# Optimization experiments

Hardware: AMD Instinct MI355X
Metric: run time of the kernel (lower is better)

The kernel has to match this reference:

```python
import jax, jax.numpy as jnp
import numpy as np

B, N, DIM, EMB_H, EXP, K = 1, 1024, 64, 64, 4, 16


def setup_inputs() -> dict:
    key = jax.random.key(0)
    ks = jax.random.split(key, 12)
    s = lambda k, *shape: jax.random.normal(k, shape, dtype=jnp.float32) * 0.05
    return {
        "x": jax.random.normal(ks[0], (B, N, DIM), dtype=jnp.float32),
        "pos": jax.random.normal(ks[1], (B, N, 3), dtype=jnp.float32),
        "Wq": s(ks[2], DIM, DIM),
        "Wk": s(ks[3], DIM, DIM),
        "Wv": s(ks[4], DIM, DIM),
        "P1": s(ks[5], 3, EMB_H), "pb1": jnp.zeros((EMB_H,), jnp.float32),
        "P2": s(ks[6], EMB_H, DIM), "pb2": jnp.zeros((DIM,), jnp.float32),
        "A1": s(ks[7], DIM, DIM * EXP), "ab1": jnp.zeros((DIM * EXP,), jnp.float32),
        "A2": s(ks[8], DIM * EXP, DIM), "ab2": jnp.zeros((DIM,), jnp.float32),
        "nneighbors": K,
    }


def reference(x, pos, Wq, Wk, Wv, P1, pb1, P2, pb2, A1, ab1, A2, ab2, nneighbors):
    b, n, d = x.shape
    q = x @ Wq            # [b,n,d]
    k = x @ Wk
    v = x @ Wv
    qk_rel = q[:, :, None, :] - k[:, None, :, :]          # [b,n,n,d]
    rel_pos = pos[:, :, None, :] - pos[:, None, :, :]      # [b,n,n,3]
    rel_pos_emb = jax.nn.relu(rel_pos @ P1 + pb1) @ P2 + pb2  # [b,n,n,d]
    # kNN selection on euclidean distance (smallest nneighbors)
    rel_dist = jnp.linalg.norm(rel_pos, axis=-1)           # [b,n,n]
    _, idx = jax.lax.top_k(-rel_dist, nneighbors)          # [b,n,K]
    bidx = jnp.arange(b)[:, None, None]
    v_g = v[bidx, idx]                                     # [b,n,K,d]
    qk_g = jnp.take_along_axis(qk_rel, idx[..., None], axis=2)        # [b,n,K,d]
    rpe_g = jnp.take_along_axis(rel_pos_emb, idx[..., None], axis=2)  # [b,n,K,d]
    v_g = v_g + rpe_g
    sim = jax.nn.relu((qk_g + rpe_g) @ A1 + ab1) @ A2 + ab2  # [b,n,K,d]
    attn = jax.nn.softmax(sim, axis=-2)                      # softmax over neighbors
    agg = jnp.sum(attn * v_g, axis=2)                        # [b,n,d]
    return agg
```

## Files before the change

### kernel.cpp

```cpp
#include <hip/hip_runtime.h>

#define NPTS 1024
#define DIMD 64
#define KNN  16
#define HID  256
#define EMBH 64

typedef short short8 __attribute__((ext_vector_type(8)));
typedef float f32x4  __attribute__((ext_vector_type(4)));

__device__ __forceinline__ short f2bf(float x) {
    unsigned u = __float_as_uint(x);
    unsigned r = (u + 0x7fffu + ((u >> 16) & 1u)) >> 16;
    return (short)r;
}
__device__ __forceinline__ float bf2f(short s) {
    return __uint_as_float(((unsigned)(unsigned short)s) << 16);
}

__device__ __host__ __forceinline__ int frag_off(int K, int k, int n) {
    int T = n >> 4, c = k >> 5, q = (k >> 3) & 3, j = k & 7;
    int lane = (q << 4) | (n & 15);
    return ((T * (K >> 5) + c) * 64 + lane) * 8 + j;
}

#define A1HI 0
#define A1LO 16384
#define A2HI 32768
#define A2LO 49152
#define WKHI 65536
#define WKLO 69632
#define WVHI 73728
#define WVLO 77824
#define P2HI 81920
#define P2LO 86016
#define WS_SHORTS 90112

__global__ __launch_bounds__(256) void prep_weights(
    const float* __restrict__ A1, const float* __restrict__ A2,
    const float* __restrict__ Wk, const float* __restrict__ Wv,
    const float* __restrict__ P2, short* __restrict__ ws)
{
    int e = blockIdx.x * 256 + threadIdx.x;
    float v; int hi_base, lo_base, off;
    if (e < 16384)      { int k = e >> 8, n = e & 255;               v = A1[e];
                          hi_base = A1HI; lo_base = A1LO; off = frag_off(64,  k, n); }
    else if (e < 32768) { int t = e - 16384; int k = t >> 6, n = t & 63; v = A2[t];
                          hi_base = A2HI; lo_base = A2LO; off = frag_off(256, k, n); }
    else if (e < 36864) { int t = e - 32768; int k = t >> 6, n = t & 63; v = Wk[t];
                          hi_base = WKHI; lo_base = WKLO; off = frag_off(64,  k, n); }
    else if (e < 40960) { int t = e - 36864; int k = t >> 6, n = t & 63; v = Wv[t];
                          hi_base = WVHI; lo_base = WVLO; off = frag_off(64,  k, n); }
    else if (e < 45056) { int t = e - 40960; int k = t >> 6, n = t & 63; v = P2[t];
                          hi_base = P2HI; lo_base = P2LO; off = frag_off(64,  k, n); }
    else return;
    short h = f2bf(v);
    short l = f2bf(v - bf2f(h));
    ws[hi_base + off] = h;
    ws[lo_base + off] = l;
}

__global__ __launch_bounds__(256, 4) void ptl_fused(
    const float* __restrict__ x,  const float* __restrict__ pos,
    const float* __restrict__ Wq,
    const float* __restrict__ P1, const float* __restrict__ pb1,
    const float* __restrict__ pb2,
    const float* __restrict__ ab1, const float* __restrict__ ab2,
    const short* __restrict__ ws,
    float* __restrict__ out)
{
    __shared__ __align__(16) float s_big[16 * 260];
    __shared__ __align__(16) float s_es[16 * 68];
    __shared__ __align__(16) float s_xn[16 * 68];
    __shared__ __align__(16) float s_h[16 * 68];
    __shared__ __align__(16) float s_vg[16 * 68];
    __shared__ float s_q[DIMD];
    __shared__ int s_idx[KNN];

    const int i   = blockIdx.x;
    const int tid = threadIdx.x;
    const int lane = tid & 63;
    const int w    = tid >> 6;
    const int q4   = lane >> 4;
    const int col  = lane & 15;

    const float px = pos[i*3+0], py = pos[i*3+1], pz = pos[i*3+2];

    #pragma unroll
    for (int u = 0; u < 4; u++) {
        int j = tid + 256 * u;
        float dx = __fsub_rn(px, pos[j*3+0]);
        float dy = __fsub_rn(py, pos[j*3+1]);
        float dz = __fsub_rn(pz, pos[j*3+2]);
        float s  = __fadd_rn(__fadd_rn(__fmul_rn(dx,dx), __fmul_rn(dy,dy)), __fmul_rn(dz,dz));
        s_big[j] = __fsqrt_rn(s);
    }
    __syncthreads();

    if (tid < 64) {
        float dist[16];
        #pragma unroll
        for (int r = 0; r < 16; r++) dist[r] = s_big[lane + 64 * r];
        for (int sel = 0; sel < KNN; sel++) {
            float mv = dist[0]; int mr = 0;
            #pragma unroll
            for (int r = 1; r < 16; r++) if (dist[r] < mv) { mv = dist[r]; mr = r; }
            int mj = lane + 64 * mr;
            #pragma unroll
            for (int off = 32; off > 0; off >>= 1) {
                float ov = __shfl_xor(mv, off);
                int   oj = __shfl_xor(mj, off);
                if (ov < mv || (ov == mv && oj < mj)) { mv = ov; mj = oj; }
            }
            if (lane == 0) s_idx[sel] = mj;
            #pragma unroll
            for (int r = 0; r < 16; r++) if (lane + 64 * r == mj) dist[r] = 3.0e38f;
        }
    } else if (tid < 128) {
        int d = tid - 64;
        const float4* xr = (const float4*)(x + i * DIMD);
        float aq = 0.f;
        #pragma unroll
        for (int cb = 0; cb < DIMD / 4; cb++) {
            float4 xv = xr[cb];
            const float* wq = Wq + (cb*4) * DIMD + d;
            aq = fmaf(xv.x, wq[0*DIMD], aq); aq = fmaf(xv.y, wq[1*DIMD], aq);
            aq = fmaf(xv.z, wq[2*DIMD], aq); aq = fmaf(xv.w, wq[3*DIMD], aq);
        }
        s_q[d] = aq;
    }
    __syncthreads();

    #pragma unroll
    for (int u = 0; u < 4; u++) {
        int t = tid + 256 * u;
        int kk = t >> 6, c = t & 63;
        s_xn[kk * 68 + c] = x[s_idx[kk] * DIMD + c];
        int j = s_idx[kk];
        float dx = px - pos[j*3+0];
        float dy = py - pos[j*3+1];
        float dz = pz - pos[j*3+2];
        float a = pb1[c];
        a = fmaf(dx, P1[0*EMBH+c], a);
        a = fmaf(dy, P1[1*EMBH+c], a);
        a = fmaf(dz, P1[2*EMBH+c], a);
        s_es[kk * 68 + c] = fmaxf(a, 0.0f);
    }
    __syncthreads();

    const short8* wsv = (const short8*)ws;

    auto build_afrag = [&](const float* row, int kbase, short8& hi, short8& lo) {
        #pragma unroll
        for (int j = 0; j < 8; j++) {
            float xv = row[kbase + j];
            short h = f2bf(xv);
            hi[j] = h;
            lo[j] = f2bf(xv - bf2f(h));
        }
    };
    auto bfrag = [&](int short_base, int f) -> short8 {
        return wsv[(short_base >> 3) + f * 64 + lane];
    };

    {
        short8 xhi[2], xlo[2], ehi[2], elo[2];
        #pragma unroll
        for (int c = 0; c < 2; c++) {
            build_afrag(s_xn + (lane & 15) * 68, 32*c + q4*8, xhi[c], xlo[c]);
            build_afrag(s_es + (lane & 15) * 68, 32*c + q4*8, ehi[c], elo[c]);
        }
        f32x4 acck = {0,0,0,0}, accv = {0,0,0,0}, accr = {0,0,0,0};
        #pragma unroll
        for (int c = 0; c < 2; c++) {
            int f = w * 2 + c;
            short8 bkh = bfrag(WKHI, f), bkl = bfrag(WKLO, f);
            short8 bvh = bfrag(WVHI, f), bvl = bfrag(WVLO, f);
            short8 bph = bfrag(P2HI, f), bpl = bfrag(P2LO, f);
            acck = __builtin_amdgcn_mfma_f32_16x16x32_bf16(xhi[c], bkh, acck, 0,0,0);
            acck = __builtin_amdgcn_mfma_f32_16x16x32_bf16(xhi[c], bkl, acck, 0,0,0);
            acck = __builtin_amdgcn_mfma_f32_16x16x32_bf16(xlo[c], bkh, acck, 0,0,0);
            accv = __builtin_amdgcn_mfma_f32_16x16x32_bf16(xhi[c], bvh, accv, 0,0,0);
            accv = __builtin_amdgcn_mfma_f32_16x16x32_bf16(xhi[c], bvl, accv, 0,0,0);
            accv = __builtin_amdgcn_mfma_f32_16x16x32_bf16(xlo[c], bvh, accv, 0,0,0);
            accr = __builtin_amdgcn_mfma_f32_16x16x32_bf16(ehi[c], bph, accr, 0,0,0);
            accr = __builtin_amdgcn_mfma_f32_16x16x32_bf16(ehi[c], bpl, accr, 0,0,0);
            accr = __builtin_amdgcn_mfma_f32_16x16x32_bf16(elo[c], bph, accr, 0,0,0);
        }
        int d = w * 16 + col;
        float qd = s_q[d], pb = pb2[d];
        #pragma unroll
        for (int r = 0; r < 4; r++) {
            int s = q4 * 4 + r;
            float rpe = accr[r] + pb;
            s_h[s * 68 + d]  = qd - acck[r] + rpe;
            s_vg[s * 68 + d] = accv[r] + rpe;
        }
    }
    __syncthreads();

    {
        short8 hhi[2], hlo[2];
        #pragma unroll
        for (int c = 0; c < 2; c++)
            build_afrag(s_h + (lane & 15) * 68, 32*c + q4*8, hhi[c], hlo[c]);
        #pragma unroll
        for (int t = 0; t < 4; t++) {
            int T = w * 4 + t;
            f32x4 acc = {0,0,0,0};
            #pragma unroll
            for (int c = 0; c < 2; c++) {
                int f = T * 2 + c;
                short8 bh = bfrag(A1HI, f), bl = bfrag(A1LO, f);
                acc = __builtin_amdgcn_mfma_f32_16x16x32_bf16(hhi[c], bh, acc, 0,0,0);
                acc = __builtin_amdgcn_mfma_f32_16x16x32_bf16(hhi[c], bl, acc, 0,0,0);
                acc = __builtin_amdgcn_mfma_f32_16x16x32_bf16(hlo[c], bh, acc, 0,0,0);
            }
            int n = T * 16 + col;
            float bias = ab1[n];
            #pragma unroll
            for (int r = 0; r < 4; r++)
                s_big[(q4 * 4 + r) * 260 + n] = fmaxf(acc[r] + bias, 0.0f);
        }
    }
    __syncthreads();

    {
        f32x4 acc = {0,0,0,0};
        #pragma unroll
        for (int c = 0; c < 8; c++) {
            short8 ahi, alo;
            build_afrag(s_big + (lane & 15) * 260, 32*c + q4*8, ahi, alo);
            int f = w * 8 + c;
            short8 bh = bfrag(A2HI, f), bl = bfrag(A2LO, f);
            acc = __builtin_amdgcn_mfma_f32_16x16x32_bf16(ahi, bh, acc, 0,0,0);
            acc = __builtin_amdgcn_mfma_f32_16x16x32_bf16(ahi, bl, acc, 0,0,0);
            acc = __builtin_amdgcn_mfma_f32_16x16x32_bf16(alo, bh, acc, 0,0,0);
        }
        int n = w * 16 + col;
        float bias = ab2[n];
        #pragma unroll
        for (int r = 0; r < 4; r++)
            s_es[(q4 * 4 + r) * 68 + n] = acc[r] + bias;
    }
    __syncthreads();

    if (tid < DIMD) {
        int d = tid;
        float mx = -3.0e38f;
        #pragma unroll
        for (int kk = 0; kk < KNN; kk++) mx = fmaxf(mx, s_es[kk * 68 + d]);
        float den = 0.0f, num = 0.0f;
        #pragma unroll
        for (int kk = 0; kk < KNN; kk++) {
            float e = expf(s_es[kk * 68 + d] - mx);
            den += e;
            num = fmaf(e, s_vg[kk * 68 + d], num);
        }
        out[i * DIMD + d] = num / den;
    }
}

extern "C" void kernel_launch(void* const* d_in, const int* in_sizes, int n_in,
                              void* d_out, int out_size, void* d_ws, size_t ws_size,
                              hipStream_t stream) {
    const float* x   = (const float*)d_in[0];
    const float* pos = (const float*)d_in[1];
    const float* Wq  = (const float*)d_in[2];
    const float* Wk  = (const float*)d_in[3];
    const float* Wv  = (const float*)d_in[4];
    const float* P1  = (const float*)d_in[5];
    const float* pb1 = (const float*)d_in[6];
    const float* P2  = (const float*)d_in[7];
    const float* pb2 = (const float*)d_in[8];
    const float* A1  = (const float*)d_in[9];
    const float* ab1 = (const float*)d_in[10];
    const float* A2  = (const float*)d_in[11];
    const float* ab2 = (const float*)d_in[12];
    float* out = (float*)d_out;
    short* ws  = (short*)d_ws;

    prep_weights<<<(45056 + 255) / 256, 256, 0, stream>>>(A1, A2, Wk, Wv, P2, ws);
    ptl_fused<<<NPTS, 256, 0, stream>>>(x, pos, Wq, P1, pb1, pb2, ab1, ab2, ws, out);
}
```

Measured before the change: 106.9 us.

## Parallelize kNN across four waves and store pre-split bf16 fragments in LDS

kNN selection now runs on all four waves: each wave picks 16 candidates from its 256 points, and wave 0 then merges the 64 candidates. This replaces a single wave scanning 16 registers per selection round. Intermediate activations are also written to LDS as hi/lo bf16 pairs in MFMA A-fragment order, so each fragment becomes one short8 vector load instead of eight scalar loads followed by conversion. Conversion moves to the producer side, which costs extra LDS stores and an extra barrier stage in the top-k.

```diff
diff --git a/kernel.cpp b/kernel.cpp
--- a/kernel.cpp
+++ b/kernel.cpp
@@ -17,6 +17,8 @@
 __device__ __forceinline__ float bf2f(short s) {
     return __uint_as_float(((unsigned)(unsigned short)s) << 16);
 }
+
+#define AOFF(k, m) ((((k) >> 3) * 16 + (m)) * 8 + ((k) & 7))
 
 __device__ __host__ __forceinline__ int frag_off(int K, int k, int n) {
     int T = n >> 4, c = k >> 5, q = (k >> 3) & 3, j = k & 7;
@@ -34,7 +36,6 @@
 #define WVLO 77824
 #define P2HI 81920
 #define P2LO 86016
-#define WS_SHORTS 90112
 
 __global__ __launch_bounds__(256) void prep_weights(
     const float* __restrict__ A1, const float* __restrict__ A2,
@@ -69,16 +70,19 @@
     const short* __restrict__ ws,
     float* __restrict__ out)
 {
-    __shared__ __align__(16) float s_big[16 * 260];
-    __shared__ __align__(16) float s_es[16 * 68];
-    __shared__ __align__(16) float s_xn[16 * 68];
-    __shared__ __align__(16) float s_h[16 * 68];
-    __shared__ __align__(16) float s_vg[16 * 68];
+    __shared__ __align__(16) short a_xn_hi[16*64],  a_xn_lo[16*64];
+    __shared__ __align__(16) short a_es_hi[16*64],  a_es_lo[16*64];
+    __shared__ __align__(16) short a_h_hi [16*64],  a_h_lo [16*64];
+    __shared__ __align__(16) short a_hd_hi[16*256], a_hd_lo[16*256];
+    __shared__ __align__(16) float s_vg[16*68];
+    __shared__ __align__(16) float s_sim[16*68];
     __shared__ float s_q[DIMD];
-    __shared__ int s_idx[KNN];
-
-    const int i   = blockIdx.x;
-    const int tid = threadIdx.x;
+    __shared__ float s_cd[64];
+    __shared__ int   s_ci[64];
+    __shared__ int   s_idx[KNN];
+
+    const int i    = blockIdx.x;
+    const int tid  = threadIdx.x;
     const int lane = tid & 63;
     const int w    = tid >> 6;
     const int q4   = lane >> 4;
@@ -86,26 +90,40 @@
 
     const float px = pos[i*3+0], py = pos[i*3+1], pz = pos[i*3+2];
 
-    #pragma unroll
-    for (int u = 0; u < 4; u++) {
-        int j = tid + 256 * u;
-        float dx = __fsub_rn(px, pos[j*3+0]);
-        float dy = __fsub_rn(py, pos[j*3+1]);
-        float dz = __fsub_rn(pz, pos[j*3+2]);
-        float s  = __fadd_rn(__fadd_rn(__fmul_rn(dx,dx), __fmul_rn(dy,dy)), __fmul_rn(dz,dz));
-        s_big[j] = __fsqrt_rn(s);
-    }
-    __syncthreads();
-
-    if (tid < 64) {
-        float dist[16];
-        #pragma unroll
-        for (int r = 0; r < 16; r++) dist[r] = s_big[lane + 64 * r];
+    {
+        const int base = w * 256;
+        float du[4];
+        #pragma unroll
+        for (int u = 0; u < 4; u++) {
+            int j = base + u * 64 + lane;
+            float dx = __fsub_rn(px, pos[j*3+0]);
+            float dy = __fsub_rn(py, pos[j*3+1]);
+            float dz = __fsub_rn(pz, pos[j*3+2]);
+            float s  = __fadd_rn(__fadd_rn(__fmul_rn(dx,dx), __fmul_rn(dy,dy)), __fmul_rn(dz,dz));
+            du[u] = __fsqrt_rn(s);
+        }
         for (int sel = 0; sel < KNN; sel++) {
-            float mv = dist[0]; int mr = 0;
-            #pragma unroll
-            for (int r = 1; r < 16; r++) if (dist[r] < mv) { mv = dist[r]; mr = r; }
-            int mj = lane + 64 * mr;
+            float mv = du[0]; int mu = 0;
+            #pragma unroll
+            for (int u = 1; u < 4; u++) if (du[u] < mv) { mv = du[u]; mu = u; }
+            int mj = base + mu * 64 + lane;
+            #pragma unroll
+            for (int off = 32; off > 0; off >>= 1) {
+                float ov = __shfl_xor(mv, off);
+                int   oj = __shfl_xor(mj, off);
+                if (ov < mv || (ov == mv && oj < mj)) { mv = ov; mj = oj; }
+            }
+            if (lane == 0) { s_cd[w * 16 + sel] = mv; s_ci[w * 16 + sel] = mj; }
+            #pragma unroll
+            for (int u = 0; u < 4; u++) if (base + u * 64 + lane == mj) du[u] = 3.0e38f;
+        }
+    }
+    __syncthreads();
+
+    if (w == 0) {
+        float md = s_cd[lane]; int mi = s_ci[lane];
+        for (int sel = 0; sel < KNN; sel++) {
+            float mv = md; int mj = mi;
             #pragma unroll
             for (int off = 32; off > 0; off >>= 1) {
                 float ov = __shfl_xor(mv, off);
@@ -113,11 +131,10 @@
                 if (ov < mv || (ov == mv && oj < mj)) { mv = ov; mj = oj; }
             }
             if (lane == 0) s_idx[sel] = mj;
-            #pragma unroll
-            for (int r = 0; r < 16; r++) if (lane + 64 * r == mj) dist[r] = 3.0e38f;
-        }
-    } else if (tid < 128) {
-        int d = tid - 64;
+            if (mi == mj) md = 3.0e38f;
+        }
+    } else if (w == 1) {
+        int d = lane;
         const float4* xr = (const float4*)(x + i * DIMD);
         float aq = 0.f;
         #pragma unroll
@@ -135,8 +152,12 @@
     for (int u = 0; u < 4; u++) {
         int t = tid + 256 * u;
         int kk = t >> 6, c = t & 63;
-        s_xn[kk * 68 + c] = x[s_idx[kk] * DIMD + c];
         int j = s_idx[kk];
+        int ao = AOFF(c, kk);
+        float xv = x[j * DIMD + c];
+        short xh = f2bf(xv);
+        a_xn_hi[ao] = xh;
+        a_xn_lo[ao] = f2bf(xv - bf2f(xh));
         float dx = px - pos[j*3+0];
         float dy = py - pos[j*3+1];
         float dz = pz - pos[j*3+2];
@@ -144,48 +165,46 @@
         a = fmaf(dx, P1[0*EMBH+c], a);
         a = fmaf(dy, P1[1*EMBH+c], a);
         a = fmaf(dz, P1[2*EMBH+c], a);
-        s_es[kk * 68 + c] = fmaxf(a, 0.0f);
-    }
-    __syncthreads();
-
-    const short8* wsv = (const short8*)ws;
-
-    auto build_afrag = [&](const float* row, int kbase, short8& hi, short8& lo) {
-        #pragma unroll
-        for (int j = 0; j < 8; j++) {
-            float xv = row[kbase + j];
-            short h = f2bf(xv);
-            hi[j] = h;
-            lo[j] = f2bf(xv - bf2f(h));
-        }
-    };
+        a = fmaxf(a, 0.0f);
+        short eh = f2bf(a);
+        a_es_hi[ao] = eh;
+        a_es_lo[ao] = f2bf(a - bf2f(eh));
+    }
+    __syncthreads();
+
+    const short8* wsv  = (const short8*)ws;
+    const short8* xnh  = (const short8*)a_xn_hi;
+    const short8* xnl  = (const short8*)a_xn_lo;
+    const short8* esh  = (const short8*)a_es_hi;
+    const short8* esl  = (const short8*)a_es_lo;
+    const short8* hhv  = (const short8*)a_h_hi;
+    const short8* hlv  = (const short8*)a_h_lo;
+    const short8* hdh  = (const short8*)a_hd_hi;
+    const short8* hdl  = (const short8*)a_hd_lo;
+
     auto bfrag = [&](int short_base, int f) -> short8 {
         return wsv[(short_base >> 3) + f * 64 + lane];
     };
 
     {
-        short8 xhi[2], xlo[2], ehi[2], elo[2];
+        f32x4 acck = {0,0,0,0}, accv = {0,0,0,0}, accr = {0,0,0,0};
         #pragma unroll
         for (int c = 0; c < 2; c++) {
-            build_afrag(s_xn + (lane & 15) * 68, 32*c + q4*8, xhi[c], xlo[c]);
-            build_afrag(s_es + (lane & 15) * 68, 32*c + q4*8, ehi[c], elo[c]);
-        }
-        f32x4 acck = {0,0,0,0}, accv = {0,0,0,0}, accr = {0,0,0,0};
-        #pragma unroll
-        for (int c = 0; c < 2; c++) {
+            int av = (4*c + q4) * 16 + col;
+            short8 xh = xnh[av], xl = xnl[av], eh = esh[av], el = esl[av];
             int f = w * 2 + c;
             short8 bkh = bfrag(WKHI, f), bkl = bfrag(WKLO, f);
             short8 bvh = bfrag(WVHI, f), bvl = bfrag(WVLO, f);
             short8 bph = bfrag(P2HI, f), bpl = bfrag(P2LO, f);
-            acck = __builtin_amdgcn_mfma_f32_16x16x32_bf16(xhi[c], bkh, acck, 0,0,0);
-            acck = __builtin_amdgcn_mfma_f32_16x16x32_bf16(xhi[c], bkl, acck, 0,0,0);
-            acck = __builtin_amdgcn_mfma_f32_16x16x32_bf16(xlo[c], bkh, acck, 0,0,0);
-            accv = __builtin_amdgcn_mfma_f32_16x16x32_bf16(xhi[c], bvh, accv, 0,0,0);
-            accv = __builtin_amdgcn_mfma_f32_16x16x32_bf16(xhi[c], bvl, accv, 0,0,0);
-            accv = __builtin_amdgcn_mfma_f32_16x16x32_bf16(xlo[c], bvh, accv, 0,0,0);
-            accr = __builtin_amdgcn_mfma_f32_16x16x32_bf16(ehi[c], bph, accr, 0,0,0);
-            accr = __builtin_amdgcn_mfma_f32_16x16x32_bf16(ehi[c], bpl, accr, 0,0,0);
-            accr = __builtin_amdgcn_mfma_f32_16x16x32_bf16(elo[c], bph, accr, 0,0,0);
+            acck = __builtin_amdgcn_mfma_f32_16x16x32_bf16(xh, bkh, acck, 0,0,0);
+            acck = __builtin_amdgcn_mfma_f32_16x16x32_bf16(xh, bkl, acck, 0,0,0);
+            acck = __builtin_amdgcn_mfma_f32_16x16x32_bf16(xl, bkh, acck, 0,0,0);
+            accv = __builtin_amdgcn_mfma_f32_16x16x32_bf16(xh, bvh, accv, 0,0,0);
+            accv = __builtin_amdgcn_mfma_f32_16x16x32_bf16(xh, bvl, accv, 0,0,0);
+            accv = __builtin_amdgcn_mfma_f32_16x16x32_bf16(xl, bvh, accv, 0,0,0);
+            accr = __builtin_amdgcn_mfma_f32_16x16x32_bf16(eh, bph, accr, 0,0,0);
+            accr = __builtin_amdgcn_mfma_f32_16x16x32_bf16(eh, bpl, accr, 0,0,0);
+            accr = __builtin_amdgcn_mfma_f32_16x16x32_bf16(el, bph, accr, 0,0,0);
         }
         int d = w * 16 + col;
         float qd = s_q[d], pb = pb2[d];
@@ -193,17 +212,23 @@
         for (int r = 0; r < 4; r++) {
             int s = q4 * 4 + r;
             float rpe = accr[r] + pb;
-            s_h[s * 68 + d]  = qd - acck[r] + rpe;
+            float hv  = qd - acck[r] + rpe;
             s_vg[s * 68 + d] = accv[r] + rpe;
+            int ao = AOFF(d, s);
+            short hh = f2bf(hv);
+            a_h_hi[ao] = hh;
+            a_h_lo[ao] = f2bf(hv - bf2f(hh));
         }
     }
     __syncthreads();
 
     {
-        short8 hhi[2], hlo[2];
-        #pragma unroll
-        for (int c = 0; c < 2; c++)
-            build_afrag(s_h + (lane & 15) * 68, 32*c + q4*8, hhi[c], hlo[c]);
+        short8 hh[2], hl[2];
+        #pragma unroll
+        for (int c = 0; c < 2; c++) {
+            int av = (4*c + q4) * 16 + col;
+            hh[c] = hhv[av]; hl[c] = hlv[av];
+        }
         #pragma unroll
         for (int t = 0; t < 4; t++) {
             int T = w * 4 + t;
@@ -212,15 +237,20 @@
             for (int c = 0; c < 2; c++) {
                 int f = T * 2 + c;
                 short8 bh = bfrag(A1HI, f), bl = bfrag(A1LO, f);
-                acc = __builtin_amdgcn_mfma_f32_16x16x32_bf16(hhi[c], bh, acc, 0,0,0);
-                acc = __builtin_amdgcn_mfma_f32_16x16x32_bf16(hhi[c], bl, acc, 0,0,0);
-                acc = __builtin_amdgcn_mfma_f32_16x16x32_bf16(hlo[c], bh, acc, 0,0,0);
+                acc = __builtin_amdgcn_mfma_f32_16x16x32_bf16(hh[c], bh, acc, 0,0,0);
+                acc = __builtin_amdgcn_mfma_f32_16x16x32_bf16(hh[c], bl, acc, 0,0,0);
+                acc = __builtin_amdgcn_mfma_f32_16x16x32_bf16(hl[c], bh, acc, 0,0,0);
             }
             int n = T * 16 + col;
             float bias = ab1[n];
             #pragma unroll
-            for (int r = 0; r < 4; r++)
-                s_big[(q4 * 4 + r) * 260 + n] = fmaxf(acc[r] + bias, 0.0f);
+            for (int r = 0; r < 4; r++) {
+                float val = fmaxf(acc[r] + bias, 0.0f);
+                int ao = AOFF(n, q4 * 4 + r);
+                short vh = f2bf(val);
+                a_hd_hi[ao] = vh;
+                a_hd_lo[ao] = f2bf(val - bf2f(vh));
+            }
         }
     }
     __syncthreads();
@@ -229,19 +259,19 @@
         f32x4 acc = {0,0,0,0};
         #pragma unroll
         for (int c = 0; c < 8; c++) {
-            short8 ahi, alo;
-            build_afrag(s_big + (lane & 15) * 260, 32*c + q4*8, ahi, alo);
+            int av = (4*c + q4) * 16 + col;
+            short8 ah = hdh[av], al = hdl[av];
             int f = w * 8 + c;
             short8 bh = bfrag(A2HI, f), bl = bfrag(A2LO, f);
-            acc = __builtin_amdgcn_mfma_f32_16x16x32_bf16(ahi, bh, acc, 0,0,0);
-            acc = __builtin_amdgcn_mfma_f32_16x16x32_bf16(ahi, bl, acc, 0,0,0);
-            acc = __builtin_amdgcn_mfma_f32_16x16x32_bf16(alo, bh, acc, 0,0,0);
+            acc = __builtin_amdgcn_mfma_f32_16x16x32_bf16(ah, bh, acc, 0,0,0);
+            acc = __builtin_amdgcn_mfma_f32_16x16x32_bf16(ah, bl, acc, 0,0,0);
+            acc = __builtin_amdgcn_mfma_f32_16x16x32_bf16(al, bh, acc, 0,0,0);
         }
         int n = w * 16 + col;
         float bias = ab2[n];
         #pragma unroll
         for (int r = 0; r < 4; r++)
-            s_es[(q4 * 4 + r) * 68 + n] = acc[r] + bias;
+            s_sim[(q4 * 4 + r) * 68 + n] = acc[r] + bias;
     }
     __syncthreads();
 
@@ -249,11 +279,11 @@
         int d = tid;
         float mx = -3.0e38f;
         #pragma unroll
-        for (int kk = 0; kk < KNN; kk++) mx = fmaxf(mx, s_es[kk * 68 + d]);
+        for (int kk = 0; kk < KNN; kk++) mx = fmaxf(mx, s_sim[kk * 68 + d]);
         float den = 0.0f, num = 0.0f;
         #pragma unroll
         for (int kk = 0; kk < KNN; kk++) {
-            float e = expf(s_es[kk * 68 + d] - mx);
+            float e = expf(s_sim[kk * 68 + d] - mx);
             den += e;
             num = fmaf(e, s_vg[kk * 68 + d], num);
         }
```

Result: slower. 110.4 us (+3.2%).
